# Optimization experiments

Hardware: AMD Instinct MI355X
Metric: run time of the kernel (lower is better)

Reference implementation:

```python
import jax, jax.numpy as jnp
import numpy as np

RANK = 8
NUM_MORPH = 10000   # morpheme vocab (num_embeddings)
CORE_DIM = 8        # ceil(512 ** (1/3))
ORDER = 3
NUM_SURF = 50000    # word vocab (num_surfaces)
EMB_DIM = 512
LN_EPS = 1e-5
BATCH, SEQ = 8, 2048


def setup_inputs() -> dict:
    key = jax.random.key(0)
    kx, kc, kw = jax.random.split(key, 3)
    # token ids over the word vocabulary
    x = jax.random.randint(kx, (BATCH, SEQ), 0, NUM_SURF, dtype=jnp.int64)
    # word -> morpheme-id mapping, one id per tensor-train order position
    co_matrix = jax.random.randint(kc, (NUM_SURF, ORDER), 0, NUM_MORPH, dtype=jnp.int64)
    # xavier_uniform over (rank, num_morph, core_dim): fan_in = num_morph*core_dim, fan_out = rank*core_dim
    bound = float(np.sqrt(6.0 / (NUM_MORPH * CORE_DIM + RANK * CORE_DIM)))
    weight = jax.random.uniform(kw, (RANK, NUM_MORPH, CORE_DIM), dtype=jnp.float32,
                                minval=-bound, maxval=bound)
    weight = weight.at[:, 0].set(0.0)  # reset_parameters zeroes morpheme index 0
    ln_scale = jnp.ones((EMB_DIM,), dtype=jnp.float32)
    ln_bias = jnp.zeros((EMB_DIM,), dtype=jnp.float32)
    return {"x": x, "co_matrix": co_matrix, "weight": weight,
            "ln_scale": ln_scale, "ln_bias": ln_bias}


def _emb_matrix(weight, co_matrix, ln_scale, ln_bias):
    # gather all order cores at once: [rank, num_surf, order, core_dim]
    cores = weight[:, co_matrix, :]
    w = cores[:, :, 0, :]                                  # [R, S, C]
    for i in range(1, ORDER):
        # order-wise broadcast outer product, flattened feature dim grows C^i
        w = (w[:, :, :, None] * cores[:, :, i, None, :]).reshape(RANK, NUM_SURF, -1)
    w = w.sum(axis=0)[:, :EMB_DIM]                         # [S, EMB_DIM]
    mu = jnp.mean(w, axis=-1, keepdims=True)
    var = jnp.var(w, axis=-1, keepdims=True)
    return (w - mu) * jax.lax.rsqrt(var + LN_EPS) * ln_scale + ln_bias


def reference(x, co_matrix, weight, ln_scale, ln_bias):
    emb = _emb_matrix(weight, co_matrix, ln_scale, ln_bias)  # full-vocab table
    return emb[x]                                            # [B, S, EMB_DIM]
```

## Files before the change

kernel.cpp:

```cpp
#include <hip/hip_runtime.h>


#define RANK      8
#define NUM_MORPH 10000
#define EMB       512
#define LN_EPS    1e-5f
#define WPB       4

__global__ __launch_bounds__(256) void morph_emb_kernel(
    const int* __restrict__ x,
    const int* __restrict__ co,
    const float* __restrict__ W,
    const float* __restrict__ lns,
    const float* __restrict__ lnb,
    float* __restrict__ out,
    int n_tok) {
    const int lane  = threadIdx.x & 63;
    const int wave  = threadIdx.x >> 6;
    const int token = blockIdx.x * WPB + wave;

    __shared__ float cbuf[WPB][3][RANK][8];

    if (token < n_tok && lane < 48) {
        const int s    = x[token];
        const int ro   = lane >> 1;
        const int o    = ro >> 3;
        const int r    = ro & 7;
        const int half = (lane & 1) << 2;
        const int m    = co[s * 3 + o];
        const float4 v = *reinterpret_cast<const float4*>(
            &W[(size_t)(r * NUM_MORPH + m) * 8 + half]);
        *reinterpret_cast<float4*>(&cbuf[wave][o][r][half]) = v;
    }
    __syncthreads();
    if (token >= n_tok) return;

    const int ia = lane >> 3;
    const int ib = lane & 7;

    float v0[4] = {0.f, 0.f, 0.f, 0.f};
    float v1[4] = {0.f, 0.f, 0.f, 0.f};
#pragma unroll
    for (int r = 0; r < RANK; ++r) {
        const float  p  = cbuf[wave][0][r][ia] * cbuf[wave][1][r][ib];
        const float4 q0 = *reinterpret_cast<const float4*>(&cbuf[wave][2][r][0]);
        const float4 q1 = *reinterpret_cast<const float4*>(&cbuf[wave][2][r][4]);
        v0[0] += p * q0.x; v0[1] += p * q0.y; v0[2] += p * q0.z; v0[3] += p * q0.w;
        v1[0] += p * q1.x; v1[1] += p * q1.y; v1[2] += p * q1.z; v1[3] += p * q1.w;
    }

    float s1 = ((v0[0] + v0[1]) + (v0[2] + v0[3])) +
               ((v1[0] + v1[1]) + (v1[2] + v1[3]));
#pragma unroll
    for (int off = 32; off > 0; off >>= 1) s1 += __shfl_xor(s1, off);
    const float mu = s1 * (1.0f / EMB);

    float d0[4], d1[4];
    float s2 = 0.f;
#pragma unroll
    for (int j = 0; j < 4; ++j) { d0[j] = v0[j] - mu; s2 += d0[j] * d0[j]; }
#pragma unroll
    for (int j = 0; j < 4; ++j) { d1[j] = v1[j] - mu; s2 += d1[j] * d1[j]; }
#pragma unroll
    for (int off = 32; off > 0; off >>= 1) s2 += __shfl_xor(s2, off);
    const float rs = rsqrtf(s2 * (1.0f / EMB) + LN_EPS);

    const int e = lane << 3;
    const float4 g0 = *reinterpret_cast<const float4*>(&lns[e]);
    const float4 g1 = *reinterpret_cast<const float4*>(&lns[e + 4]);
    const float4 b0 = *reinterpret_cast<const float4*>(&lnb[e]);
    const float4 b1 = *reinterpret_cast<const float4*>(&lnb[e + 4]);

    float4 o0, o1;
    o0.x = d0[0] * rs * g0.x + b0.x;
    o0.y = d0[1] * rs * g0.y + b0.y;
    o0.z = d0[2] * rs * g0.z + b0.z;
    o0.w = d0[3] * rs * g0.w + b0.w;
    o1.x = d1[0] * rs * g1.x + b1.x;
    o1.y = d1[1] * rs * g1.y + b1.y;
    o1.z = d1[2] * rs * g1.z + b1.z;
    o1.w = d1[3] * rs * g1.w + b1.w;

    float* op = out + (size_t)token * EMB + e;
    *reinterpret_cast<float4*>(op)     = o0;
    *reinterpret_cast<float4*>(op + 4) = o1;
}

extern "C" void kernel_launch(void* const* d_in, const int* in_sizes, int n_in,
                              void* d_out, int out_size, void* d_ws, size_t ws_size,
                              hipStream_t stream) {
    const int*   x   = (const int*)d_in[0];
    const int*   co  = (const int*)d_in[1];
    const float* W   = (const float*)d_in[2];
    const float* lns = (const float*)d_in[3];
    const float* lnb = (const float*)d_in[4];
    float*       out = (float*)d_out;

    const int n_tok  = in_sizes[0];
    const int blocks = (n_tok + WPB - 1) / WPB;
    morph_emb_kernel<<<blocks, WPB * 64, 0, stream>>>(x, co, W, lns, lnb, out, n_tok);
}
```

Baseline: 16.89 us.

## Load cores directly from global memory, two tokens per wave, single-pass LayerNorm

Removes the LDS staging buffer and __syncthreads, so each lane reads its tensor-train core values directly from global memory (mostly broadcast or cached loads). Each wave now processes two tokens, which raises memory-level parallelism and halves the block count. LayerNorm statistics are computed in one pass as sum and sum of squares, removing one shuffle-reduction round. This risks lower precision in the variance, more redundant per-lane global loads, and fewer waves in flight.

```diff
diff --git a/kernel.cpp b/kernel.cpp
--- a/kernel.cpp
+++ b/kernel.cpp
@@ -5,7 +5,9 @@
 #define NUM_MORPH 10000
 #define EMB       512
 #define LN_EPS    1e-5f
+#define STRIDE_R  (NUM_MORPH * 8)
 #define WPB       4
+#define TPW       2
 
 __global__ __launch_bounds__(256) void morph_emb_kernel(
     const int* __restrict__ x,
@@ -15,75 +17,101 @@
     const float* __restrict__ lnb,
     float* __restrict__ out,
     int n_tok) {
-    const int lane  = threadIdx.x & 63;
-    const int wave  = threadIdx.x >> 6;
-    const int token = blockIdx.x * WPB + wave;
+    const int lane = threadIdx.x & 63;
+    const int wid  = blockIdx.x * WPB + (threadIdx.x >> 6);
+    const int t0   = wid * TPW;
+    if (t0 >= n_tok) return;
+    const bool has1 = (t0 + 1) < n_tok;
 
-    __shared__ float cbuf[WPB][3][RANK][8];
+    const int s0 = x[t0];
+    const int s1 = has1 ? x[t0 + 1] : s0;
 
-    if (token < n_tok && lane < 48) {
-        const int s    = x[token];
-        const int ro   = lane >> 1;
-        const int o    = ro >> 3;
-        const int r    = ro & 7;
-        const int half = (lane & 1) << 2;
-        const int m    = co[s * 3 + o];
-        const float4 v = *reinterpret_cast<const float4*>(
-            &W[(size_t)(r * NUM_MORPH + m) * 8 + half]);
-        *reinterpret_cast<float4*>(&cbuf[wave][o][r][half]) = v;
-    }
-    __syncthreads();
-    if (token >= n_tok) return;
+    const int m00 = co[s0 * 3],     m01 = co[s0 * 3 + 1], m02 = co[s0 * 3 + 2];
+    const int m10 = co[s1 * 3],     m11 = co[s1 * 3 + 1], m12 = co[s1 * 3 + 2];
 
     const int ia = lane >> 3;
     const int ib = lane & 7;
 
-    float v0[4] = {0.f, 0.f, 0.f, 0.f};
-    float v1[4] = {0.f, 0.f, 0.f, 0.f};
+    const float* pa0 = W + m00 * 8 + ia;
+    const float* pb0 = W + m01 * 8 + ib;
+    const float* pc0 = W + m02 * 8;
+    const float* pa1 = W + m10 * 8 + ia;
+    const float* pb1 = W + m11 * 8 + ib;
+    const float* pc1 = W + m12 * 8;
+
+    float acc0[8] = {0,0,0,0,0,0,0,0};
+    float acc1[8] = {0,0,0,0,0,0,0,0};
+
 #pragma unroll
     for (int r = 0; r < RANK; ++r) {
-        const float  p  = cbuf[wave][0][r][ia] * cbuf[wave][1][r][ib];
-        const float4 q0 = *reinterpret_cast<const float4*>(&cbuf[wave][2][r][0]);
-        const float4 q1 = *reinterpret_cast<const float4*>(&cbuf[wave][2][r][4]);
-        v0[0] += p * q0.x; v0[1] += p * q0.y; v0[2] += p * q0.z; v0[3] += p * q0.w;
-        v1[0] += p * q1.x; v1[1] += p * q1.y; v1[2] += p * q1.z; v1[3] += p * q1.w;
+        const int ro = r * STRIDE_R;
+        const float  p0  = pa0[ro] * pb0[ro];
+        const float4 q00 = *reinterpret_cast<const float4*>(pc0 + ro);
+        const float4 q01 = *reinterpret_cast<const float4*>(pc0 + ro + 4);
+        const float  p1  = pa1[ro] * pb1[ro];
+        const float4 q10 = *reinterpret_cast<const float4*>(pc1 + ro);
+        const float4 q11 = *reinterpret_cast<const float4*>(pc1 + ro + 4);
+        acc0[0] += p0 * q00.x; acc0[1] += p0 * q00.y;
+        acc0[2] += p0 * q00.z; acc0[3] += p0 * q00.w;
+        acc0[4] += p0 * q01.x; acc0[5] += p0 * q01.y;
+        acc0[6] += p0 * q01.z; acc0[7] += p0 * q01.w;
+        acc1[0] += p1 * q10.x; acc1[1] += p1 * q10.y;
+        acc1[2] += p1 * q10.z; acc1[3] += p1 * q10.w;
+        acc1[4] += p1 * q11.x; acc1[5] += p1 * q11.y;
+        acc1[6] += p1 * q11.z; acc1[7] += p1 * q11.w;
     }
 
-    float s1 = ((v0[0] + v0[1]) + (v0[2] + v0[3])) +
-               ((v1[0] + v1[1]) + (v1[2] + v1[3]));
+    float sA = 0.f, qA = 0.f, sB = 0.f, qB = 0.f;
 #pragma unroll
-    for (int off = 32; off > 0; off >>= 1) s1 += __shfl_xor(s1, off);
-    const float mu = s1 * (1.0f / EMB);
-
-    float d0[4], d1[4];
-    float s2 = 0.f;
+    for (int j = 0; j < 8; ++j) {
+        sA += acc0[j]; qA += acc0[j] * acc0[j];
+        sB += acc1[j]; qB += acc1[j] * acc1[j];
+    }
 #pragma unroll
-    for (int j = 0; j < 4; ++j) { d0[j] = v0[j] - mu; s2 += d0[j] * d0[j]; }
-#pragma unroll
-    for (int j = 0; j < 4; ++j) { d1[j] = v1[j] - mu; s2 += d1[j] * d1[j]; }
-#pragma unroll
-    for (int off = 32; off > 0; off >>= 1) s2 += __shfl_xor(s2, off);
-    const float rs = rsqrtf(s2 * (1.0f / EMB) + LN_EPS);
+    for (int off = 32; off > 0; off >>= 1) {
+        sA += __shfl_xor(sA, off); qA += __shfl_xor(qA, off);
+        sB += __shfl_xor(sB, off); qB += __shfl_xor(qB, off);
+    }
+    const float muA = sA * (1.0f / EMB);
+    const float muB = sB * (1.0f / EMB);
+    const float rsA = rsqrtf(qA * (1.0f / EMB) - muA * muA + LN_EPS);
+    const float rsB = rsqrtf(qB * (1.0f / EMB) - muB * muB + LN_EPS);
 
     const int e = lane << 3;
     const float4 g0 = *reinterpret_cast<const float4*>(&lns[e]);
     const float4 g1 = *reinterpret_cast<const float4*>(&lns[e + 4]);
     const float4 b0 = *reinterpret_cast<const float4*>(&lnb[e]);
     const float4 b1 = *reinterpret_cast<const float4*>(&lnb[e + 4]);
+    const float gv[8] = {g0.x, g0.y, g0.z, g0.w, g1.x, g1.y, g1.z, g1.w};
+    const float bv[8] = {b0.x, b0.y, b0.z, b0.w, b1.x, b1.y, b1.z, b1.w};
 
-    float4 o0, o1;
-    o0.x = d0[0] * rs * g0.x + b0.x;
-    o0.y = d0[1] * rs * g0.y + b0.y;
-    o0.z = d0[2] * rs * g0.z + b0.z;
-    o0.w = d0[3] * rs * g0.w + b0.w;
-    o1.x = d1[0] * rs * g1.x + b1.x;
-    o1.y = d1[1] * rs * g1.y + b1.y;
-    o1.z = d1[2] * rs * g1.z + b1.z;
-    o1.w = d1[3] * rs * g1.w + b1.w;
+    float4 oA0, oA1;
+    oA0.x = (acc0[0] - muA) * rsA * gv[0] + bv[0];
+    oA0.y = (acc0[1] - muA) * rsA * gv[1] + bv[1];
+    oA0.z = (acc0[2] - muA) * rsA * gv[2] + bv[2];
+    oA0.w = (acc0[3] - muA) * rsA * gv[3] + bv[3];
+    oA1.x = (acc0[4] - muA) * rsA * gv[4] + bv[4];
+    oA1.y = (acc0[5] - muA) * rsA * gv[5] + bv[5];
+    oA1.z = (acc0[6] - muA) * rsA * gv[6] + bv[6];
+    oA1.w = (acc0[7] - muA) * rsA * gv[7] + bv[7];
+    float* opA = out + (size_t)t0 * EMB + e;
+    *reinterpret_cast<float4*>(opA)     = oA0;
+    *reinterpret_cast<float4*>(opA + 4) = oA1;
 
-    float* op = out + (size_t)token * EMB + e;
-    *reinterpret_cast<float4*>(op)     = o0;
-    *reinterpret_cast<float4*>(op + 4) = o1;
+    if (has1) {
+        float4 oB0, oB1;
+        oB0.x = (acc1[0] - muB) * rsB * gv[0] + bv[0];
+        oB0.y = (acc1[1] - muB) * rsB * gv[1] + bv[1];
+        oB0.z = (acc1[2] - muB) * rsB * gv[2] + bv[2];
+        oB0.w = (acc1[3] - muB) * rsB * gv[3] + bv[3];
+        oB1.x = (acc1[4] - muB) * rsB * gv[4] + bv[4];
+        oB1.y = (acc1[5] - muB) * rsB * gv[5] + bv[5];
+        oB1.z = (acc1[6] - muB) * rsB * gv[6] + bv[6];
+        oB1.w = (acc1[7] - muB) * rsB * gv[7] + bv[7];
+        float* opB = out + (size_t)(t0 + 1) * EMB + e;
+        *reinterpret_cast<float4*>(opB)     = oB0;
+        *reinterpret_cast<float4*>(opB + 4) = oB1;
+    }
 }
 
 extern "C" void kernel_launch(void* const* d_in, const int* in_sizes, int n_in,
@@ -97,6 +125,7 @@
     float*       out = (float*)d_out;
 
     const int n_tok  = in_sizes[0];
-    const int blocks = (n_tok + WPB - 1) / WPB;
+    const int tok_per_block = WPB * TPW;
+    const int blocks = (n_tok + tok_per_block - 1) / tok_per_block;
     morph_emb_kernel<<<blocks, WPB * 64, 0, stream>>>(x, co, W, lns, lnb, out, n_tok);
 }
```

After: 21.89 us. +29.6%, slower.

## Process four tokens per wavefront with cooperative gather and single-pass LayerNorm stats

Applied to the files above, without the earlier changes.

Each wavefront now handles four tokens instead of one. All 64 lanes share the gather of the core vectors for the four tokens through three float4 load rounds, and the LayerNorm scale and bias loads are amortized across the tokens. The mean and variance reductions are fused into one shuffle pass using sum and sum of squares, so the four tokens' reductions can interleave and hide shuffle latency. This cuts block count and per-token overhead, but raises register pressure and uses the less numerically robust E[x²]−μ² variance. Waves past n_tok now return before __syncthreads, which could misbehave on partial tail blocks.

```diff
diff --git a/kernel.cpp b/kernel.cpp
--- a/kernel.cpp
+++ b/kernel.cpp
@@ -6,6 +6,7 @@
 #define EMB       512
 #define LN_EPS    1e-5f
 #define WPB       4
+#define TPW       4
 
 __global__ __launch_bounds__(256) void morph_emb_kernel(
     const int* __restrict__ x,
@@ -17,73 +18,98 @@
     int n_tok) {
     const int lane  = threadIdx.x & 63;
     const int wave  = threadIdx.x >> 6;
-    const int token = blockIdx.x * WPB + wave;
+    const int tbase = (blockIdx.x * WPB + wave) * TPW;
+    if (tbase >= n_tok) return;
 
-    __shared__ float cbuf[WPB][3][RANK][8];
+    __shared__ float cbuf[WPB][TPW][3][RANK][8];
 
-    if (token < n_tok && lane < 48) {
-        const int s    = x[token];
-        const int ro   = lane >> 1;
-        const int o    = ro >> 3;
-        const int r    = ro & 7;
-        const int half = (lane & 1) << 2;
-        const int m    = co[s * 3 + o];
+    int s_ld = 0;
+    if (lane < TPW) {
+        int tt = tbase + lane;
+        if (tt >= n_tok) tt = n_tok - 1;
+        s_ld = x[tt];
+    }
+
+#pragma unroll
+    for (int q = 0; q < 3; ++q) {
+        const int f    = q * 64 + lane;
+        const int t    = f / 48;
+        const int ff   = f - t * 48;
+        const int row  = ff >> 1;
+        const int o    = row >> 3;
+        const int r    = row & 7;
+        const int half = (ff & 1) << 2;
+        const int s_t  = __shfl(s_ld, t);
+        const int m    = co[s_t * 3 + o];
         const float4 v = *reinterpret_cast<const float4*>(
             &W[(size_t)(r * NUM_MORPH + m) * 8 + half]);
-        *reinterpret_cast<float4*>(&cbuf[wave][o][r][half]) = v;
+        *reinterpret_cast<float4*>(&cbuf[wave][t][o][r][half]) = v;
     }
-    __syncthreads();
-    if (token >= n_tok) return;
-
-    const int ia = lane >> 3;
-    const int ib = lane & 7;
-
-    float v0[4] = {0.f, 0.f, 0.f, 0.f};
-    float v1[4] = {0.f, 0.f, 0.f, 0.f};
-#pragma unroll
-    for (int r = 0; r < RANK; ++r) {
-        const float  p  = cbuf[wave][0][r][ia] * cbuf[wave][1][r][ib];
-        const float4 q0 = *reinterpret_cast<const float4*>(&cbuf[wave][2][r][0]);
-        const float4 q1 = *reinterpret_cast<const float4*>(&cbuf[wave][2][r][4]);
-        v0[0] += p * q0.x; v0[1] += p * q0.y; v0[2] += p * q0.z; v0[3] += p * q0.w;
-        v1[0] += p * q1.x; v1[1] += p * q1.y; v1[2] += p * q1.z; v1[3] += p * q1.w;
-    }
-
-    float s1 = ((v0[0] + v0[1]) + (v0[2] + v0[3])) +
-               ((v1[0] + v1[1]) + (v1[2] + v1[3]));
-#pragma unroll
-    for (int off = 32; off > 0; off >>= 1) s1 += __shfl_xor(s1, off);
-    const float mu = s1 * (1.0f / EMB);
-
-    float d0[4], d1[4];
-    float s2 = 0.f;
-#pragma unroll
-    for (int j = 0; j < 4; ++j) { d0[j] = v0[j] - mu; s2 += d0[j] * d0[j]; }
-#pragma unroll
-    for (int j = 0; j < 4; ++j) { d1[j] = v1[j] - mu; s2 += d1[j] * d1[j]; }
-#pragma unroll
-    for (int off = 32; off > 0; off >>= 1) s2 += __shfl_xor(s2, off);
-    const float rs = rsqrtf(s2 * (1.0f / EMB) + LN_EPS);
 
     const int e = lane << 3;
     const float4 g0 = *reinterpret_cast<const float4*>(&lns[e]);
     const float4 g1 = *reinterpret_cast<const float4*>(&lns[e + 4]);
     const float4 b0 = *reinterpret_cast<const float4*>(&lnb[e]);
     const float4 b1 = *reinterpret_cast<const float4*>(&lnb[e + 4]);
+    const float gv[8] = {g0.x, g0.y, g0.z, g0.w, g1.x, g1.y, g1.z, g1.w};
+    const float bv[8] = {b0.x, b0.y, b0.z, b0.w, b1.x, b1.y, b1.z, b1.w};
 
-    float4 o0, o1;
-    o0.x = d0[0] * rs * g0.x + b0.x;
-    o0.y = d0[1] * rs * g0.y + b0.y;
-    o0.z = d0[2] * rs * g0.z + b0.z;
-    o0.w = d0[3] * rs * g0.w + b0.w;
-    o1.x = d1[0] * rs * g1.x + b1.x;
-    o1.y = d1[1] * rs * g1.y + b1.y;
-    o1.z = d1[2] * rs * g1.z + b1.z;
-    o1.w = d1[3] * rs * g1.w + b1.w;
+    __syncthreads();
 
-    float* op = out + (size_t)token * EMB + e;
-    *reinterpret_cast<float4*>(op)     = o0;
-    *reinterpret_cast<float4*>(op + 4) = o1;
+    const int ia = lane >> 3;
+    const int ib = lane & 7;
+
+    float acc[TPW][8] = {};
+#pragma unroll
+    for (int r = 0; r < RANK; ++r) {
+#pragma unroll
+        for (int t = 0; t < TPW; ++t) {
+            const float  p  = cbuf[wave][t][0][r][ia] * cbuf[wave][t][1][r][ib];
+            const float4 q0 = *reinterpret_cast<const float4*>(&cbuf[wave][t][2][r][0]);
+            const float4 q1 = *reinterpret_cast<const float4*>(&cbuf[wave][t][2][r][4]);
+            acc[t][0] += p * q0.x; acc[t][1] += p * q0.y;
+            acc[t][2] += p * q0.z; acc[t][3] += p * q0.w;
+            acc[t][4] += p * q1.x; acc[t][5] += p * q1.y;
+            acc[t][6] += p * q1.z; acc[t][7] += p * q1.w;
+        }
+    }
+
+    float sm[TPW], sq[TPW];
+#pragma unroll
+    for (int t = 0; t < TPW; ++t) {
+        float s = 0.f, q = 0.f;
+#pragma unroll
+        for (int j = 0; j < 8; ++j) { s += acc[t][j]; q += acc[t][j] * acc[t][j]; }
+        sm[t] = s; sq[t] = q;
+    }
+#pragma unroll
+    for (int off = 32; off > 0; off >>= 1) {
+#pragma unroll
+        for (int t = 0; t < TPW; ++t) {
+            sm[t] += __shfl_xor(sm[t], off);
+            sq[t] += __shfl_xor(sq[t], off);
+        }
+    }
+
+#pragma unroll
+    for (int t = 0; t < TPW; ++t) {
+        if (tbase + t < n_tok) {
+            const float mu = sm[t] * (1.0f / EMB);
+            const float rs = rsqrtf(sq[t] * (1.0f / EMB) - mu * mu + LN_EPS);
+            float4 o0, o1;
+            o0.x = (acc[t][0] - mu) * rs * gv[0] + bv[0];
+            o0.y = (acc[t][1] - mu) * rs * gv[1] + bv[1];
+            o0.z = (acc[t][2] - mu) * rs * gv[2] + bv[2];
+            o0.w = (acc[t][3] - mu) * rs * gv[3] + bv[3];
+            o1.x = (acc[t][4] - mu) * rs * gv[4] + bv[4];
+            o1.y = (acc[t][5] - mu) * rs * gv[5] + bv[5];
+            o1.z = (acc[t][6] - mu) * rs * gv[6] + bv[6];
+            o1.w = (acc[t][7] - mu) * rs * gv[7] + bv[7];
+            float* op = out + (size_t)(tbase + t) * EMB + e;
+            *reinterpret_cast<float4*>(op)     = o0;
+            *reinterpret_cast<float4*>(op + 4) = o1;
+        }
+    }
 }
 
 extern "C" void kernel_launch(void* const* d_in, const int* in_sizes, int n_in,
@@ -96,7 +122,8 @@
     const float* lnb = (const float*)d_in[4];
     float*       out = (float*)d_out;
 
-    const int n_tok  = in_sizes[0];
-    const int blocks = (n_tok + WPB - 1) / WPB;
+    const int n_tok = in_sizes[0];
+    const int tok_per_block = WPB * TPW;
+    const int blocks = (n_tok + tok_per_block - 1) / tok_per_block;
     morph_emb_kernel<<<blocks, WPB * 64, 0, stream>>>(x, co, W, lns, lnb, out, n_tok);
 }
```

Measured after the change: 18.20 us. 1.08x slower.
